# Kernel optimization log

Measured on AMD Instinct MI355X. Metric: run time of the kernel, lower is better.

Reference implementation:

```python
import jax, jax.numpy as jnp
import numpy as np

TOP_K = 2  # top_routing

def setup_inputs() -> dict:
    key = jax.random.key(0)
    ks = jax.random.split(key, 8)
    B, D, O, E = 2048, 1024, 1024, 8
    H = D * 10  # hidden_dim hard-coded as input_dim*10
    s_d = 1.0 / np.sqrt(D)
    s_h = 1.0 / np.sqrt(H)
    return {
        "x1": jax.random.normal(ks[0], (B, D), jnp.float32),
        "x2": jax.random.normal(ks[1], (B, D), jnp.float32),
        "gate_w": jax.random.uniform(ks[2], (E, D), jnp.float32, -s_d, s_d),
        "gate_b": jax.random.uniform(ks[3], (E,), jnp.float32, -s_d, s_d),
        "fc1_w": jax.random.uniform(ks[4], (E, H, D), jnp.float32, -s_d, s_d),
        "fc1_b": jax.random.uniform(ks[5], (E, H), jnp.float32, -s_d, s_d),
        "fc2_w": jax.random.uniform(ks[6], (E, O, H), jnp.float32, -s_h, s_h),
        "fc2_b": jax.random.uniform(ks[7], (E, O), jnp.float32, -s_h, s_h),
    }


def reference(x1, x2, gate_w, gate_b, fc1_w, fc1_b, fc2_w, fc2_b):
    # Gate: softmax over experts, then top-k sparsify (values kept, rest zeroed)
    gate_logits = x1 @ gate_w.T + gate_b                    # [B, E]
    gate_probs = jax.nn.softmax(gate_logits, axis=1)
    top_vals, top_idx = jax.lax.top_k(gate_probs, TOP_K)    # [B, K]
    B = gate_probs.shape[0]
    rows = jnp.arange(B)[:, None]
    gate_probs = jnp.zeros_like(gate_probs).at[rows, top_idx].set(top_vals)

    # All experts run densely on x2 (faithful to the original Python loop)
    hidden = jnp.einsum('bd,ehd->beh', x2, fc1_w) + fc1_b   # [B, E, H]
    hidden = jax.nn.relu(hidden)
    expert_out = jnp.einsum('beh,eoh->beo', hidden, fc2_w) + fc2_b  # [B, E, O]

    # bmm(gate_probs[:,None,:], expert_out).squeeze(1)
    return jnp.einsum('be,beo->bo', gate_probs, expert_out)  # [B, O]
```

## Files before the change

### kernel.cpp

```cpp
#include <hip/hip_runtime.h>
#include <hip/hip_fp16.h>
#include <stdint.h>

#define BTOK 2048
#define DIM 1024
#define ODIM 1024
#define NEXP 8
#define HID 10240
#define CAP 2048
#define KSPL 4

typedef _Float16 half8 __attribute__((ext_vector_type(8)));
typedef __fp16 fp16x2 __attribute__((ext_vector_type(2)));
typedef float floatx4 __attribute__((ext_vector_type(4)));

#define WS_HIDDEN_OFF 0
#define WS_COUNTS_OFF 83886080UL
#define WS_TOKENS_OFF 83886144UL
#define WS_PROBS_OFF  83951680UL
#define WS_NEEDED     84017216UL

typedef __attribute__((address_space(1))) const unsigned int guint;
typedef __attribute__((address_space(3))) unsigned int luint;
__device__ __forceinline__ void gload16(const void* g, void* l) {
    __builtin_amdgcn_global_load_lds((guint*)g, (luint*)l, 16, 0, 0);
}

__global__ void gate_kernel(const float* __restrict__ x1,
                            const float* __restrict__ gate_w,
                            const float* __restrict__ gate_b,
                            int* counts, int* tokens, float* probs) {
    int b = blockIdx.x;
    int lane = threadIdx.x;
    const float* xr = x1 + (size_t)b * DIM;
    float acc[NEXP];
#pragma unroll
    for (int e = 0; e < NEXP; e++) acc[e] = 0.f;
    for (int i = 0; i < DIM / 64; i++) {
        int d = lane + i * 64;
        float xv = xr[d];
#pragma unroll
        for (int e = 0; e < NEXP; e++) acc[e] += xv * gate_w[e * DIM + d];
    }
#pragma unroll
    for (int e = 0; e < NEXP; e++)
        for (int off = 32; off > 0; off >>= 1) acc[e] += __shfl_xor(acc[e], off);
    if (lane == 0) {
        float l[NEXP], m = -1e30f;
#pragma unroll
        for (int e = 0; e < NEXP; e++) { l[e] = acc[e] + gate_b[e]; m = fmaxf(m, l[e]); }
        float p[NEXP], s = 0.f;
#pragma unroll
        for (int e = 0; e < NEXP; e++) { p[e] = expf(l[e] - m); s += p[e]; }
        float inv = 1.f / s;
        int e0 = 0; float v0 = p[0];
#pragma unroll
        for (int e = 1; e < NEXP; e++) if (p[e] > v0) { v0 = p[e]; e0 = e; }
        int e1 = -1; float v1 = -1.f;
#pragma unroll
        for (int e = 0; e < NEXP; e++) if (e != e0 && p[e] > v1) { v1 = p[e]; e1 = e; }
        int pos0 = atomicAdd(&counts[e0], 1);
        tokens[e0 * CAP + pos0] = b; probs[e0 * CAP + pos0] = v0 * inv;
        int pos1 = atomicAdd(&counts[e1], 1);
        tokens[e1 * CAP + pos1] = b; probs[e1 * CAP + pos1] = v1 * inv;
    }
}

__global__ void offsets_kernel(const int* counts, int* offs) {
    if (threadIdx.x == 0) {
        int r = 0;
        for (int e = 0; e < NEXP; e++) { offs[e] = r; r += counts[e]; }
    }
}

#define BM 128
#define BN 128
#define BK 32

__device__ __forceinline__ half8 cvt8(float4 a, float4 b) {
    union { fp16x2 h2[4]; half8 h8; } u;
    u.h2[0] = __builtin_amdgcn_cvt_pkrtz(a.x, a.y);
    u.h2[1] = __builtin_amdgcn_cvt_pkrtz(a.z, a.w);
    u.h2[2] = __builtin_amdgcn_cvt_pkrtz(b.x, b.y);
    u.h2[3] = __builtin_amdgcn_cvt_pkrtz(b.z, b.w);
    return u.h8;
}

__global__ __launch_bounds__(256, 3) void gemm1_kernel(
    const float* __restrict__ x2, const float* __restrict__ fc1_w,
    const float* __restrict__ fc1_b, const int* __restrict__ counts,
    const int* __restrict__ offs, const int* __restrict__ tokens,
    _Float16* __restrict__ hidden) {
    int d = blockIdx.x;
    int logical = (d & 7) * (gridDim.x >> 3) + (d >> 3);
    int mt = logical & 15;
    int rest = logical >> 4;
    int nt = rest % (HID / BN);
    int e = rest / (HID / BN);

    int cnt = counts[e];
    int m0 = mt * BM;
    if (m0 >= cnt) return;
    int n0 = nt * BN;
    int off = offs[e];

    __shared__ __align__(16) float As[BM * BK];
    __shared__ __align__(16) float Bs[BN * BK];

    int t = threadIdx.x, lane = t & 63, wave = t >> 6;
    int waveM = wave & 1, waveN = wave >> 1;

    int srow = t >> 3;
    int sg = (t & 7) ^ (srow & 7);
    const char* abase[4];
#pragma unroll
    for (int i = 0; i < 4; i++) {
        int row = i * 32 + srow;
        int arow = min(m0 + row, cnt - 1);
        int tok = tokens[e * CAP + arow];
        abase[i] = (const char*)(x2 + (size_t)tok * DIM + sg * 4);
    }
    const char* bbase = (const char*)(fc1_w + ((size_t)e * HID + n0 + srow) * DIM + sg * 4);
    char* asd = (char*)As + wave * 1024;
    char* bsd = (char*)Bs + wave * 1024;

    floatx4 acc[4][4];
#pragma unroll
    for (int mi = 0; mi < 4; mi++)
#pragma unroll
        for (int ni = 0; ni < 4; ni++) acc[mi][ni] = (floatx4){0.f, 0.f, 0.f, 0.f};

    int fr = lane & 15, q = lane >> 4;
#pragma unroll
    for (int i = 0; i < 4; i++) {
        gload16(abase[i], asd + i * 4096);
        gload16(bbase + i * (32 * DIM * 4), bsd + i * 4096);
    }
    const int KT = DIM / BK;
    for (int kt = 0; kt < KT; kt++) {
        __syncthreads();
        half8 af[4], bf[4];
#pragma unroll
        for (int mi = 0; mi < 4; mi++) {
            int row = waveM * 64 + mi * 16 + fr;
            float4 f0 = *(const float4*)((const char*)As + row * 128 + ((2 * q) ^ (row & 7)) * 16);
            float4 f1 = *(const float4*)((const char*)As + row * 128 + ((2 * q + 1) ^ (row & 7)) * 16);
            af[mi] = cvt8(f0, f1);
        }
#pragma unroll
        for (int ni = 0; ni < 4; ni++) {
            int row = waveN * 64 + ni * 16 + fr;
            float4 f0 = *(const float4*)((const char*)Bs + row * 128 + ((2 * q) ^ (row & 7)) * 16);
            float4 f1 = *(const float4*)((const char*)Bs + row * 128 + ((2 * q + 1) ^ (row & 7)) * 16);
            bf[ni] = cvt8(f0, f1);
        }
        __syncthreads();
        if (kt + 1 < KT) {
            int koff = (kt + 1) * 128;
#pragma unroll
            for (int i = 0; i < 4; i++) {
                gload16(abase[i] + koff, asd + i * 4096);
                gload16(bbase + i * (32 * DIM * 4) + koff, bsd + i * 4096);
            }
        }
#pragma unroll
        for (int mi = 0; mi < 4; mi++)
#pragma unroll
            for (int ni = 0; ni < 4; ni++)
                acc[mi][ni] = __builtin_amdgcn_mfma_f32_16x16x32_f16(
                    af[mi], bf[ni], acc[mi][ni], 0, 0, 0);
    }
#pragma unroll
    for (int ni = 0; ni < 4; ni++) {
        int col = n0 + waveN * 64 + ni * 16 + fr;
        float bias = fc1_b[e * HID + col];
#pragma unroll
        for (int mi = 0; mi < 4; mi++) {
#pragma unroll
            for (int r = 0; r < 4; r++) {
                int rl = m0 + waveM * 64 + mi * 16 + q * 4 + r;
                if (rl < cnt) {
                    float v = fmaxf(acc[mi][ni][r] + bias, 0.f);
                    hidden[(size_t)(off + rl) * HID + col] = (_Float16)v;
                }
            }
        }
    }
}

__global__ __launch_bounds__(256, 3) void gemm2_kernel(
    const _Float16* __restrict__ hidden, const float* __restrict__ fc2_w,
    const float* __restrict__ fc2_b, const int* __restrict__ counts,
    const int* __restrict__ offs, const int* __restrict__ tokens,
    const float* __restrict__ probs, float* __restrict__ out) {
    int d = blockIdx.x;
    int logical = (d & 7) * (gridDim.x >> 3) + (d >> 3);
    int mt = logical & 15;
    int rest = logical >> 4;
    int nt = rest & 7;
    int rest2 = rest >> 3;
    int ks = rest2 & (KSPL - 1);
    int e = rest2 >> 2;

    int cnt = counts[e];
    int m0 = mt * BM;
    if (m0 >= cnt) return;
    int n0 = nt * BN;
    int off = offs[e];
    int k0 = ks * (HID / KSPL);

    __shared__ __align__(16) _Float16 Ash[BM * BK];
    __shared__ __align__(16) float Bs[BN * BK];

    int t = threadIdx.x, lane = t & 63, wave = t >> 6;
    int waveM = wave & 1, waveN = wave >> 1;

    int sarow = t >> 2;
    int sag = (t & 3) ^ ((sarow >> 1) & 3);
    const char* abase[2];
#pragma unroll
    for (int i = 0; i < 2; i++) {
        int row = i * 64 + sarow;
        int arow = min(m0 + row, cnt - 1);
        abase[i] = (const char*)(hidden + (size_t)(off + arow) * HID + k0 + sag * 8);
    }
    int sbrow = t >> 3;
    int sbg = (t & 7) ^ (sbrow & 7);
    const char* bbase = (const char*)(fc2_w + ((size_t)e * ODIM + n0 + sbrow) * HID + k0 + sbg * 4);
    char* asd = (char*)Ash + wave * 1024;
    char* bsd = (char*)Bs + wave * 1024;

    floatx4 acc[4][4];
#pragma unroll
    for (int mi = 0; mi < 4; mi++)
#pragma unroll
        for (int ni = 0; ni < 4; ni++) acc[mi][ni] = (floatx4){0.f, 0.f, 0.f, 0.f};

    int fr = lane & 15, q = lane >> 4;
#pragma unroll
    for (int i = 0; i < 2; i++) gload16(abase[i], asd + i * 4096);
#pragma unroll
    for (int i = 0; i < 4; i++) gload16(bbase + i * (32 * HID * 4), bsd + i * 4096);

    const int KT = (HID / KSPL) / BK;
    for (int kt = 0; kt < KT; kt++) {
        __syncthreads();
        half8 af[4], bf[4];
#pragma unroll
        for (int mi = 0; mi < 4; mi++) {
            int row = waveM * 64 + mi * 16 + fr;
            af[mi] = *(const half8*)((const char*)Ash + row * 64 + (q ^ ((row >> 1) & 3)) * 16);
        }
#pragma unroll
        for (int ni = 0; ni < 4; ni++) {
            int row = waveN * 64 + ni * 16 + fr;
            float4 f0 = *(const float4*)((const char*)Bs + row * 128 + ((2 * q) ^ (row & 7)) * 16);
            float4 f1 = *(const float4*)((const char*)Bs + row * 128 + ((2 * q + 1) ^ (row & 7)) * 16);
            bf[ni] = cvt8(f0, f1);
        }
        __syncthreads();
        if (kt + 1 < KT) {
            int koffA = (kt + 1) * 64;
            int koffB = (kt + 1) * 128;
#pragma unroll
            for (int i = 0; i < 2; i++) gload16(abase[i] + koffA, asd + i * 4096);
#pragma unroll
            for (int i = 0; i < 4; i++) gload16(bbase + i * (32 * HID * 4) + koffB, bsd + i * 4096);
        }
#pragma unroll
        for (int mi = 0; mi < 4; mi++)
#pragma unroll
            for (int ni = 0; ni < 4; ni++)
                acc[mi][ni] = __builtin_amdgcn_mfma_f32_16x16x32_f16(
                    af[mi], bf[ni], acc[mi][ni], 0, 0, 0);
    }
#pragma unroll
    for (int ni = 0; ni < 4; ni++) {
        int col = n0 + waveN * 64 + ni * 16 + fr;
        float bias = (ks == 0) ? fc2_b[e * ODIM + col] : 0.f;
#pragma unroll
        for (int mi = 0; mi < 4; mi++) {
#pragma unroll
            for (int r = 0; r < 4; r++) {
                int rl = m0 + waveM * 64 + mi * 16 + q * 4 + r;
                if (rl < cnt) {
                    float p = probs[e * CAP + rl];
                    int tok = tokens[e * CAP + rl];
                    atomicAdd(&out[(size_t)tok * ODIM + col],
                              p * (acc[mi][ni][r] + bias));
                }
            }
        }
    }
}

extern "C" void kernel_launch(void* const* d_in, const int* in_sizes, int n_in,
                              void* d_out, int out_size, void* d_ws, size_t ws_size,
                              hipStream_t stream) {
    if (ws_size < WS_NEEDED) return;
    const float* x1 = (const float*)d_in[0];
    const float* x2 = (const float*)d_in[1];
    const float* gate_w = (const float*)d_in[2];
    const float* gate_b = (const float*)d_in[3];
    const float* fc1_w = (const float*)d_in[4];
    const float* fc1_b = (const float*)d_in[5];
    const float* fc2_w = (const float*)d_in[6];
    const float* fc2_b = (const float*)d_in[7];
    float* out = (float*)d_out;
    char* ws = (char*)d_ws;
    _Float16* hidden = (_Float16*)(ws + WS_HIDDEN_OFF);
    int* counts = (int*)(ws + WS_COUNTS_OFF);
    int* offs = counts + NEXP;
    int* tokens = (int*)(ws + WS_TOKENS_OFF);
    float* probs = (float*)(ws + WS_PROBS_OFF);

    (void)hipMemsetAsync(counts, 0, 2 * NEXP * sizeof(int), stream);
    (void)hipMemsetAsync(d_out, 0, (size_t)out_size * sizeof(float), stream);
    gate_kernel<<<BTOK, 64, 0, stream>>>(x1, gate_w, gate_b, counts, tokens, probs);
    offsets_kernel<<<1, 64, 0, stream>>>(counts, offs);
    gemm1_kernel<<<(CAP / BM) * (HID / BN) * NEXP, 256, 0, stream>>>(
        x2, fc1_w, fc1_b, counts, offs, tokens, hidden);
    gemm2_kernel<<<(CAP / BM) * (ODIM / BN) * NEXP * KSPL, 256, 0, stream>>>(
        hidden, fc2_w, fc2_b, counts, offs, tokens, probs, out);
}
```

Measured before the change: 1.272 ms.

## Enlarge GEMM tiles to 256x256 with register-staged fp16 LDS double buffering

```diff
diff --git a/kernel.cpp b/kernel.cpp
--- a/kernel.cpp
+++ b/kernel.cpp
@@ -8,7 +8,7 @@
 #define NEXP 8
 #define HID 10240
 #define CAP 2048
-#define KSPL 4
+#define KSPL 8
 
 typedef _Float16 half8 __attribute__((ext_vector_type(8)));
 typedef __fp16 fp16x2 __attribute__((ext_vector_type(2)));
@@ -19,12 +19,6 @@
 #define WS_TOKENS_OFF 83886144UL
 #define WS_PROBS_OFF  83951680UL
 #define WS_NEEDED     84017216UL
-
-typedef __attribute__((address_space(1))) const unsigned int guint;
-typedef __attribute__((address_space(3))) unsigned int luint;
-__device__ __forceinline__ void gload16(const void* g, void* l) {
-    __builtin_amdgcn_global_load_lds((guint*)g, (luint*)l, 16, 0, 0);
-}
 
 __global__ void gate_kernel(const float* __restrict__ x1,
                             const float* __restrict__ gate_w,
@@ -73,8 +67,8 @@
     }
 }
 
-#define BM 128
-#define BN 128
+#define BM 256
+#define BN 256
 #define BK 32
 
 __device__ __forceinline__ half8 cvt8(float4 a, float4 b) {
@@ -86,17 +80,16 @@
     return u.h8;
 }
 
-__global__ __launch_bounds__(256, 3) void gemm1_kernel(
+__global__ __launch_bounds__(1024, 4) void gemm1_kernel(
     const float* __restrict__ x2, const float* __restrict__ fc1_w,
     const float* __restrict__ fc1_b, const int* __restrict__ counts,
     const int* __restrict__ offs, const int* __restrict__ tokens,
     _Float16* __restrict__ hidden) {
     int d = blockIdx.x;
-    int logical = (d & 7) * (gridDim.x >> 3) + (d >> 3);
-    int mt = logical & 15;
-    int rest = logical >> 4;
-    int nt = rest % (HID / BN);
-    int e = rest / (HID / BN);
+    int e = d & 7;
+    int rest = d >> 3;
+    int nt = rest >> 3;
+    int mt = rest & 7;
 
     int cnt = counts[e];
     int m0 = mt * BM;
@@ -104,25 +97,22 @@
     int n0 = nt * BN;
     int off = offs[e];
 
-    __shared__ __align__(16) float As[BM * BK];
-    __shared__ __align__(16) float Bs[BN * BK];
-
-    int t = threadIdx.x, lane = t & 63, wave = t >> 6;
-    int waveM = wave & 1, waveN = wave >> 1;
-
-    int srow = t >> 3;
-    int sg = (t & 7) ^ (srow & 7);
-    const char* abase[4];
-#pragma unroll
-    for (int i = 0; i < 4; i++) {
-        int row = i * 32 + srow;
-        int arow = min(m0 + row, cnt - 1);
-        int tok = tokens[e * CAP + arow];
-        abase[i] = (const char*)(x2 + (size_t)tok * DIM + sg * 4);
-    }
-    const char* bbase = (const char*)(fc1_w + ((size_t)e * HID + n0 + srow) * DIM + sg * 4);
-    char* asd = (char*)As + wave * 1024;
-    char* bsd = (char*)Bs + wave * 1024;
+    __shared__ __align__(16) _Float16 As[2 * BM * BK];
+    __shared__ __align__(16) _Float16 Bs[2 * BN * BK];
+
+    int t = threadIdx.x;
+    int lane = t & 63, wave = t >> 6;
+    int waveM = wave >> 2, waveN = wave & 3;
+    int fr = lane & 15, q = lane >> 4;
+
+    int srow = t >> 2;
+    int sg = t & 3;
+    int swz = sg ^ ((srow >> 1) & 3);
+    int arow = min(m0 + srow, cnt - 1);
+    const float* ag = x2 + (size_t)tokens[e * CAP + arow] * DIM + sg * 8;
+    const float* bg = fc1_w + ((size_t)e * HID + n0 + srow) * DIM + sg * 8;
+    _Float16* aw = As + srow * BK + swz * 8;
+    _Float16* bw = Bs + srow * BK + swz * 8;
 
     floatx4 acc[4][4];
 #pragma unroll
@@ -130,45 +120,50 @@
 #pragma unroll
         for (int ni = 0; ni < 4; ni++) acc[mi][ni] = (floatx4){0.f, 0.f, 0.f, 0.f};
 
-    int fr = lane & 15, q = lane >> 4;
-#pragma unroll
-    for (int i = 0; i < 4; i++) {
-        gload16(abase[i], asd + i * 4096);
-        gload16(bbase + i * (32 * DIM * 4), bsd + i * 4096);
-    }
+    float4 pa0, pa1, pb0, pb1;
+    auto LOADT = [&](int kt) {
+        const float* a_ = ag + kt * BK;
+        const float* b_ = bg + kt * BK;
+        pa0 = *(const float4*)a_;
+        pa1 = *(const float4*)(a_ + 4);
+        pb0 = *(const float4*)b_;
+        pb1 = *(const float4*)(b_ + 4);
+    };
+    auto WRITET = [&](int buf) {
+        *(half8*)(aw + buf * (BM * BK)) = cvt8(pa0, pa1);
+        *(half8*)(bw + buf * (BN * BK)) = cvt8(pb0, pb1);
+    };
+
     const int KT = DIM / BK;
+    LOADT(0);
+    WRITET(0);
+    LOADT(1);
+    __syncthreads();
+    int cur = 0;
     for (int kt = 0; kt < KT; kt++) {
-        __syncthreads();
         half8 af[4], bf[4];
+        const _Float16* Ar = As + cur * (BM * BK);
+        const _Float16* Br = Bs + cur * (BN * BK);
 #pragma unroll
         for (int mi = 0; mi < 4; mi++) {
             int row = waveM * 64 + mi * 16 + fr;
-            float4 f0 = *(const float4*)((const char*)As + row * 128 + ((2 * q) ^ (row & 7)) * 16);
-            float4 f1 = *(const float4*)((const char*)As + row * 128 + ((2 * q + 1) ^ (row & 7)) * 16);
-            af[mi] = cvt8(f0, f1);
+            af[mi] = *(const half8*)(Ar + row * BK + ((q ^ ((row >> 1) & 3)) * 8));
         }
 #pragma unroll
         for (int ni = 0; ni < 4; ni++) {
             int row = waveN * 64 + ni * 16 + fr;
-            float4 f0 = *(const float4*)((const char*)Bs + row * 128 + ((2 * q) ^ (row & 7)) * 16);
-            float4 f1 = *(const float4*)((const char*)Bs + row * 128 + ((2 * q + 1) ^ (row & 7)) * 16);
-            bf[ni] = cvt8(f0, f1);
-        }
-        __syncthreads();
-        if (kt + 1 < KT) {
-            int koff = (kt + 1) * 128;
-#pragma unroll
-            for (int i = 0; i < 4; i++) {
-                gload16(abase[i] + koff, asd + i * 4096);
-                gload16(bbase + i * (32 * DIM * 4) + koff, bsd + i * 4096);
-            }
-        }
+            bf[ni] = *(const half8*)(Br + row * BK + ((q ^ ((row >> 1) & 3)) * 8));
+        }
+        if (kt + 1 < KT) WRITET(cur ^ 1);
+        if (kt + 2 < KT) LOADT(kt + 2);
 #pragma unroll
         for (int mi = 0; mi < 4; mi++)
 #pragma unroll
             for (int ni = 0; ni < 4; ni++)
                 acc[mi][ni] = __builtin_amdgcn_mfma_f32_16x16x32_f16(
                     af[mi], bf[ni], acc[mi][ni], 0, 0, 0);
+        __syncthreads();
+        cur ^= 1;
     }
 #pragma unroll
     for (int ni = 0; ni < 4; ni++) {
@@ -188,19 +183,17 @@
     }
 }
 
-__global__ __launch_bounds__(256, 3) void gemm2_kernel(
+__global__ __launch_bounds__(1024, 4) void gemm2_kernel(
     const _Float16* __restrict__ hidden, const float* __restrict__ fc2_w,
     const float* __restrict__ fc2_b, const int* __restrict__ counts,
     const int* __restrict__ offs, const int* __restrict__ tokens,
     const float* __restrict__ probs, float* __restrict__ out) {
     int d = blockIdx.x;
-    int logical = (d & 7) * (gridDim.x >> 3) + (d >> 3);
-    int mt = logical & 15;
-    int rest = logical >> 4;
-    int nt = rest & 7;
-    int rest2 = rest >> 3;
-    int ks = rest2 & (KSPL - 1);
-    int e = rest2 >> 2;
+    int e = d & 7;
+    int rest = d >> 3;
+    int mt = rest & 7;
+    int nt = (rest >> 3) & 3;
+    int ks = rest >> 5;
 
     int cnt = counts[e];
     int m0 = mt * BM;
@@ -209,26 +202,22 @@
     int off = offs[e];
     int k0 = ks * (HID / KSPL);
 
-    __shared__ __align__(16) _Float16 Ash[BM * BK];
-    __shared__ __align__(16) float Bs[BN * BK];
-
-    int t = threadIdx.x, lane = t & 63, wave = t >> 6;
-    int waveM = wave & 1, waveN = wave >> 1;
-
-    int sarow = t >> 2;
-    int sag = (t & 3) ^ ((sarow >> 1) & 3);
-    const char* abase[2];
-#pragma unroll
-    for (int i = 0; i < 2; i++) {
-        int row = i * 64 + sarow;
-        int arow = min(m0 + row, cnt - 1);
-        abase[i] = (const char*)(hidden + (size_t)(off + arow) * HID + k0 + sag * 8);
-    }
-    int sbrow = t >> 3;
-    int sbg = (t & 7) ^ (sbrow & 7);
-    const char* bbase = (const char*)(fc2_w + ((size_t)e * ODIM + n0 + sbrow) * HID + k0 + sbg * 4);
-    char* asd = (char*)Ash + wave * 1024;
-    char* bsd = (char*)Bs + wave * 1024;
+    __shared__ __align__(16) _Float16 As[2 * BM * BK];
+    __shared__ __align__(16) _Float16 Bs[2 * BN * BK];
+
+    int t = threadIdx.x;
+    int lane = t & 63, wave = t >> 6;
+    int waveM = wave >> 2, waveN = wave & 3;
+    int fr = lane & 15, q = lane >> 4;
+
+    int srow = t >> 2;
+    int sg = t & 3;
+    int swz = sg ^ ((srow >> 1) & 3);
+    int arow = min(m0 + srow, cnt - 1);
+    const _Float16* ag = hidden + (size_t)(off + arow) * HID + k0 + sg * 8;
+    const float* bg = fc2_w + ((size_t)e * ODIM + n0 + srow) * HID + k0 + sg * 8;
+    _Float16* aw = As + srow * BK + swz * 8;
+    _Float16* bw = Bs + srow * BK + swz * 8;
 
     floatx4 acc[4][4];
 #pragma unroll
@@ -236,43 +225,49 @@
 #pragma unroll
         for (int ni = 0; ni < 4; ni++) acc[mi][ni] = (floatx4){0.f, 0.f, 0.f, 0.f};
 
-    int fr = lane & 15, q = lane >> 4;
-#pragma unroll
-    for (int i = 0; i < 2; i++) gload16(abase[i], asd + i * 4096);
-#pragma unroll
-    for (int i = 0; i < 4; i++) gload16(bbase + i * (32 * HID * 4), bsd + i * 4096);
+    half8 pa;
+    float4 pb0, pb1;
+    auto LOADT = [&](int kt) {
+        pa = *(const half8*)(ag + kt * BK);
+        const float* b_ = bg + kt * BK;
+        pb0 = *(const float4*)b_;
+        pb1 = *(const float4*)(b_ + 4);
+    };
+    auto WRITET = [&](int buf) {
+        *(half8*)(aw + buf * (BM * BK)) = pa;
+        *(half8*)(bw + buf * (BN * BK)) = cvt8(pb0, pb1);
+    };
 
     const int KT = (HID / KSPL) / BK;
+    LOADT(0);
+    WRITET(0);
+    LOADT(1);
+    __syncthreads();
+    int cur = 0;
     for (int kt = 0; kt < KT; kt++) {
-        __syncthreads();
         half8 af[4], bf[4];
+        const _Float16* Ar = As + cur * (BM * BK);
+        const _Float16* Br = Bs + cur * (BN * BK);
 #pragma unroll
         for (int mi = 0; mi < 4; mi++) {
             int row = waveM * 64 + mi * 16 + fr;
-            af[mi] = *(const half8*)((const char*)Ash + row * 64 + (q ^ ((row >> 1) & 3)) * 16);
+            af[mi] = *(const half8*)(Ar + row * BK + ((q ^ ((row >> 1) & 3)) * 8));
         }
 #pragma unroll
         for (int ni = 0; ni < 4; ni++) {
             int row = waveN * 64 + ni * 16 + fr;
-            float4 f0 = *(const float4*)((const char*)Bs + row * 128 + ((2 * q) ^ (row & 7)) * 16);
-            float4 f1 = *(const float4*)((const char*)Bs + row * 128 + ((2 * q + 1) ^ (row & 7)) * 16);
-            bf[ni] = cvt8(f0, f1);
-        }
-        __syncthreads();
-        if (kt + 1 < KT) {
-            int koffA = (kt + 1) * 64;
-            int koffB = (kt + 1) * 128;
-#pragma unroll
-            for (int i = 0; i < 2; i++) gload16(abase[i] + koffA, asd + i * 4096);
-#pragma unroll
-            for (int i = 0; i < 4; i++) gload16(bbase + i * (32 * HID * 4) + koffB, bsd + i * 4096);
-        }
+            bf[ni] = *(const half8*)(Br + row * BK + ((q ^ ((row >> 1) & 3)) * 8));
+        }
+        if (kt + 1 < KT) WRITET(cur ^ 1);
+        if (kt + 2 < KT) LOADT(kt + 2);
 #pragma unroll
         for (int mi = 0; mi < 4; mi++)
 #pragma unroll
             for (int ni = 0; ni < 4; ni++)
                 acc[mi][ni] = __builtin_amdgcn_mfma_f32_16x16x32_f16(
                     af[mi], bf[ni], acc[mi][ni], 0, 0, 0);
+        __syncthreads();
+        cur ^= 1;
     }
 #pragma unroll
     for (int ni = 0; ni < 4; ni++) {
@@ -318,8 +313,8 @@
     (void)hipMemsetAsync(d_out, 0, (size_t)out_size * sizeof(float), stream);
     gate_kernel<<<BTOK, 64, 0, stream>>>(x1, gate_w, gate_b, counts, tokens, probs);
     offsets_kernel<<<1, 64, 0, stream>>>(counts, offs);
-    gemm1_kernel<<<(CAP / BM) * (HID / BN) * NEXP, 256, 0, stream>>>(
+    gemm1_kernel<<<(CAP / BM) * (HID / BN) * NEXP, 1024, 0, stream>>>(
         x2, fc1_w, fc1_b, counts, offs, tokens, hidden);
-    gemm2_kernel<<<(CAP / BM) * (ODIM / BN) * NEXP * KSPL, 256, 0, stream>>>(
+    gemm2_kernel<<<(CAP / BM) * (ODIM / BN) * NEXP * KSPL, 1024, 0, stream>>>(
         hidden, fc2_w, fc2_b, counts, offs, tokens, probs, out);
 }
```

Result: faster. 1.160 ms (-8.8%).
